# Performance work log

Hardware: AMD Instinct MI355X
Metric: run time of the kernel (lower is better)

## Reference

```python
import jax, jax.numpy as jnp
import numpy as np

N_NODES = 100000
N_EDGES = 1600000
F_IN = 128
HID = 128
N_CLASSES = 32
N_GRAPHS = 512


def _seg_mean(vals, idx, num_segments):
    s = jax.ops.segment_sum(vals, idx, num_segments=num_segments)
    cnt = jax.ops.segment_sum(jnp.ones((vals.shape[0],), vals.dtype), idx, num_segments=num_segments)
    return s / jnp.maximum(cnt, 1.0)[:, None]


def _sage_conv(x, src, dst, Wl, bl, Wr):
    # PyG SAGEConv(mean): out = lin_l(mean_{j in N(i)} x_j) + lin_r(x_i); lin_l has bias, lin_r does not.
    agg = _seg_mean(x[src], dst, N_NODES)          # gather + scatter-mean  [N, d]
    return agg @ Wl.T + bl + x @ Wr.T              # [N, H]


def setup_inputs() -> dict:
    key = jax.random.key(0)
    ks = jax.random.split(key, 16)
    x = jax.random.normal(ks[0], (N_NODES, F_IN), dtype=jnp.float32)
    edge_index = jax.random.randint(ks[1], (2, N_EDGES), 0, N_NODES, dtype=jnp.int64)
    batch = jnp.sort(jax.random.randint(ks[2], (N_NODES,), 0, N_GRAPHS, dtype=jnp.int64))
    sc = 0.05
    params = {
        'Wl0': jax.random.normal(ks[3], (HID, F_IN), jnp.float32) * sc,
        'bl0': jnp.zeros((HID,), jnp.float32),
        'Wr0': jax.random.normal(ks[4], (HID, F_IN), jnp.float32) * sc,
        'Wl1': jax.random.normal(ks[5], (HID, HID), jnp.float32) * sc,
        'bl1': jnp.zeros((HID,), jnp.float32),
        'Wr1': jax.random.normal(ks[6], (HID, HID), jnp.float32) * sc,
        'Wl2': jax.random.normal(ks[7], (HID, HID), jnp.float32) * sc,
        'bl2': jnp.zeros((HID,), jnp.float32),
        'Wr2': jax.random.normal(ks[8], (HID, HID), jnp.float32) * sc,
        'Wlin': jax.random.normal(ks[9], (N_CLASSES, HID), jnp.float32) * sc,
        'blin': jnp.zeros((N_CLASSES,), jnp.float32),
    }
    return {'x': x, 'edge_index': edge_index, 'batch': batch, **params}


def reference(x, edge_index, batch, Wl0, bl0, Wr0, Wl1, bl1, Wr1, Wl2, bl2, Wr2, Wlin, blin):
    src, dst = edge_index[0], edge_index[1]
    # GraphSAGE backbone: relu between layers, no act after last (out_channels set); dropout=identity in eval.
    h = jax.nn.relu(_sage_conv(x, src, dst, Wl0, bl0, Wr0))
    h = jax.nn.relu(_sage_conv(h, src, dst, Wl1, bl1, Wr1))
    h = _sage_conv(h, src, dst, Wl2, bl2, Wr2)
    # global_mean_pool over batch index -> [n_graphs, HID]
    g = _seg_mean(h, batch, N_GRAPHS)
    return g @ Wlin.T + blin  # [n_graphs, n_classes]
```

## Files before the change

kernel.cpp:

```cpp
#include <hip/hip_runtime.h>
#include <hip/hip_bf16.h>


typedef __attribute__((ext_vector_type(8))) short short8v;
typedef __attribute__((ext_vector_type(4))) float f32x4;

__device__ __forceinline__ unsigned short f2bf(float f) {
    __hip_bfloat16 h = __float2bfloat16(f);
    return *reinterpret_cast<unsigned short*>(&h);
}
__device__ __forceinline__ float bf_lo(unsigned u) { return __uint_as_float(u << 16); }
__device__ __forceinline__ float bf_hi(unsigned u) { return __uint_as_float(u & 0xffff0000u); }
__device__ __forceinline__ unsigned packbf(float lo, float hi) {
    return ((unsigned)f2bf(hi) << 16) | f2bf(lo);
}


__global__ void rank_kernel(const int* __restrict__ dst, int* __restrict__ cnt,
                            unsigned short* __restrict__ rank, int nE) {
    int e = blockIdx.x * blockDim.x + threadIdx.x;
    if (e < nE) {
        int r = atomicAdd(&cnt[dst[e]], 1);
        rank[e] = (unsigned short)r;
    }
}

__global__ void scan1_kernel(const int* __restrict__ deg, int* __restrict__ rowptr,
                             int* __restrict__ bsum, int n) {
    __shared__ int s[1024];
    int lid = threadIdx.x;
    int i = blockIdx.x * 1024 + lid;
    int v = (i < n) ? deg[i] : 0;
    s[lid] = v;
    __syncthreads();
    #pragma unroll
    for (int off = 1; off < 1024; off <<= 1) {
        int t = (lid >= off) ? s[lid - off] : 0;
        __syncthreads();
        s[lid] += t;
        __syncthreads();
    }
    if (i < n) rowptr[i] = s[lid] - v;
    if (lid == 0) bsum[blockIdx.x] = s[1023];
}

__global__ void scan2_kernel(int* __restrict__ bsum, int nb) {
    __shared__ int s[1024];
    int lid = threadIdx.x;
    int v = (lid < nb) ? bsum[lid] : 0;
    s[lid] = v;
    __syncthreads();
    #pragma unroll
    for (int off = 1; off < 1024; off <<= 1) {
        int t = (lid >= off) ? s[lid - off] : 0;
        __syncthreads();
        s[lid] += t;
        __syncthreads();
    }
    if (lid < nb) bsum[lid] = s[lid] - v;
}

__global__ void scan3_kernel(int* __restrict__ rowptr, const int* __restrict__ bsum,
                             int n, int nE) {
    int i = blockIdx.x * blockDim.x + threadIdx.x;
    if (i < n) rowptr[i] += bsum[i >> 10];
    if (i == 0) rowptr[n] = nE;
}

__global__ void scatter_rank_kernel(const int* __restrict__ src, const int* __restrict__ dst,
                                    const unsigned short* __restrict__ rank,
                                    const int* __restrict__ rowptr,
                                    int* __restrict__ esrc, int nE, int lo, int hi) {
    int e = blockIdx.x * blockDim.x + threadIdx.x;
    if (e < nE) {
        int d = dst[e];
        if (d >= lo && d < hi) {
            esrc[rowptr[d] + (int)rank[e]] = src[e];
        }
    }
}


__global__ void cvt_kernel(const float* __restrict__ in, unsigned short* __restrict__ out, int n4) {
    int i = blockIdx.x * blockDim.x + threadIdx.x;
    if (i < n4) {
        float4 v = ((const float4*)in)[i];
        ushort4 o;
        o.x = f2bf(v.x); o.y = f2bf(v.y); o.z = f2bf(v.z); o.w = f2bf(v.w);
        ((ushort4*)out)[i] = o;
    }
}

__global__ void cvt6_kernel(const float* __restrict__ w0, const float* __restrict__ w1,
                            const float* __restrict__ w2, const float* __restrict__ w3,
                            const float* __restrict__ w4, const float* __restrict__ w5,
                            unsigned short* __restrict__ o0, unsigned short* __restrict__ o1,
                            unsigned short* __restrict__ o2, unsigned short* __restrict__ o3,
                            unsigned short* __restrict__ o4, unsigned short* __restrict__ o5,
                            int n4) {
    const float* in; unsigned short* out;
    switch (blockIdx.y) {
        case 0: in = w0; out = o0; break;
        case 1: in = w1; out = o1; break;
        case 2: in = w2; out = o2; break;
        case 3: in = w3; out = o3; break;
        case 4: in = w4; out = o4; break;
        default: in = w5; out = o5; break;
    }
    int i = blockIdx.x * blockDim.x + threadIdx.x;
    if (i < n4) {
        float4 v = ((const float4*)in)[i];
        ushort4 o;
        o.x = f2bf(v.x); o.y = f2bf(v.y); o.z = f2bf(v.z); o.w = f2bf(v.w);
        ((ushort4*)out)[i] = o;
    }
}


__global__ void aggregate_kernel(const unsigned short* __restrict__ h,
                                 const int* __restrict__ rowptr,
                                 const int* __restrict__ esrc,
                                 unsigned short* __restrict__ agg, int n) {
    int wave = (blockIdx.x * blockDim.x + threadIdx.x) >> 6;
    int lane = threadIdx.x & 63;
    if (wave >= n) return;
    int beg = rowptr[wave], end = rowptr[wave + 1];
    int q  = lane >> 4;
    int c0 = (lane & 15) * 8;
    float s0=0.f,s1=0.f,s2=0.f,s3=0.f,s4=0.f,s5=0.f,s6=0.f,s7=0.f;
    int j = beg + q;
    for (; j + 4 < end; j += 8) {
        int r0 = esrc[j], r1 = esrc[j + 4];
        uint4 v0 = *(const uint4*)&h[(size_t)r0 * 128 + c0];
        uint4 v1 = *(const uint4*)&h[(size_t)r1 * 128 + c0];
        s0 += bf_lo(v0.x); s1 += bf_hi(v0.x); s2 += bf_lo(v0.y); s3 += bf_hi(v0.y);
        s4 += bf_lo(v0.z); s5 += bf_hi(v0.z); s6 += bf_lo(v0.w); s7 += bf_hi(v0.w);
        s0 += bf_lo(v1.x); s1 += bf_hi(v1.x); s2 += bf_lo(v1.y); s3 += bf_hi(v1.y);
        s4 += bf_lo(v1.z); s5 += bf_hi(v1.z); s6 += bf_lo(v1.w); s7 += bf_hi(v1.w);
    }
    if (j < end) {
        int r0 = esrc[j];
        uint4 v0 = *(const uint4*)&h[(size_t)r0 * 128 + c0];
        s0 += bf_lo(v0.x); s1 += bf_hi(v0.x); s2 += bf_lo(v0.y); s3 += bf_hi(v0.y);
        s4 += bf_lo(v0.z); s5 += bf_hi(v0.z); s6 += bf_lo(v0.w); s7 += bf_hi(v0.w);
    }
    s0 += __shfl_xor(s0, 16); s0 += __shfl_xor(s0, 32);
    s1 += __shfl_xor(s1, 16); s1 += __shfl_xor(s1, 32);
    s2 += __shfl_xor(s2, 16); s2 += __shfl_xor(s2, 32);
    s3 += __shfl_xor(s3, 16); s3 += __shfl_xor(s3, 32);
    s4 += __shfl_xor(s4, 16); s4 += __shfl_xor(s4, 32);
    s5 += __shfl_xor(s5, 16); s5 += __shfl_xor(s5, 32);
    s6 += __shfl_xor(s6, 16); s6 += __shfl_xor(s6, 32);
    s7 += __shfl_xor(s7, 16); s7 += __shfl_xor(s7, 32);
    if (lane < 16) {
        int cnt = end - beg;
        float inv = 1.0f / (float)(cnt > 1 ? cnt : 1);
        uint4 o;
        o.x = packbf(s0 * inv, s1 * inv);
        o.y = packbf(s2 * inv, s3 * inv);
        o.z = packbf(s4 * inv, s5 * inv);
        o.w = packbf(s6 * inv, s7 * inv);
        *(uint4*)&agg[(size_t)wave * 128 + c0] = o;
    }
}


__launch_bounds__(256)
__global__ void sage_gemm_mfma(const unsigned short* __restrict__ A,
                               const unsigned short* __restrict__ H,
                               const unsigned short* __restrict__ Wl,
                               const unsigned short* __restrict__ Wr,
                               const float* __restrict__ bl,
                               unsigned short* __restrict__ out, int n, int relu) {
    int tid  = threadIdx.x;
    int lane = tid & 63;
    int w    = tid >> 6;
    int wm   = w >> 1, wn = w & 1;
    int br   = blockIdx.x * 128 + wm * 64;
    int bc   = wn * 64;
    int lrow = lane & 15;
    int lk   = (lane >> 4) * 8;

    f32x4 acc[4][4] = {};

    #pragma unroll
    for (int half = 0; half < 2; ++half) {
        const unsigned short* X = half ? H : A;
        const unsigned short* W = half ? Wr : Wl;
        const unsigned short* xp[4];
        const unsigned short* wp[4];
        #pragma unroll
        for (int mb = 0; mb < 4; ++mb) {
            int r = br + mb * 16 + lrow;
            if (r >= n) r = n - 1;
            xp[mb] = X + (size_t)r * 128 + lk;
        }
        #pragma unroll
        for (int nb = 0; nb < 4; ++nb)
            wp[nb] = W + (size_t)(bc + nb * 16 + lrow) * 128 + lk;

        #pragma unroll
        for (int ks = 0; ks < 4; ++ks) {
            short8v a[4], b[4];
            #pragma unroll
            for (int mb = 0; mb < 4; ++mb) a[mb] = *(const short8v*)(xp[mb] + ks * 32);
            #pragma unroll
            for (int nb = 0; nb < 4; ++nb) b[nb] = *(const short8v*)(wp[nb] + ks * 32);
            #pragma unroll
            for (int mb = 0; mb < 4; ++mb)
                #pragma unroll
                for (int nb = 0; nb < 4; ++nb)
                    acc[mb][nb] = __builtin_amdgcn_mfma_f32_16x16x32_bf16(
                        a[mb], b[nb], acc[mb][nb], 0, 0, 0);
        }
    }

    int ccol  = lane & 15;
    int crow4 = (lane >> 4) * 4;
    float bv[4];
    #pragma unroll
    for (int nb = 0; nb < 4; ++nb) bv[nb] = bl[bc + nb * 16 + ccol];

    #pragma unroll
    for (int mb = 0; mb < 4; ++mb) {
        #pragma unroll
        for (int r = 0; r < 4; ++r) {
            int row = br + mb * 16 + crow4 + r;
            if (row < n) {
                #pragma unroll
                for (int nb = 0; nb < 4; ++nb) {
                    int col = bc + nb * 16 + ccol;
                    float v = acc[mb][nb][r] + bv[nb];
                    if (relu && v < 0.f) v = 0.f;
                    out[(size_t)row * 128 + col] = f2bf(v);
                }
            }
        }
    }
}


__device__ __forceinline__ int lbound(const int* __restrict__ a, int n, int v) {
    int lo = 0, hi = n;
    while (lo < hi) { int m = (lo + hi) >> 1; if (a[m] < v) lo = m + 1; else hi = m; }
    return lo;
}

__launch_bounds__(1024)
__global__ void pool_kernel(const unsigned short* __restrict__ h, const int* __restrict__ batch,
                            float* __restrict__ g, int n) {
    __shared__ float red[16][128];
    int b  = blockIdx.x;
    int rg = threadIdx.x >> 6;
    int cp = threadIdx.x & 63;
    int lo = lbound(batch, n, b);
    int hi = lbound(batch, n, b + 1);
    float s0 = 0.f, s1 = 0.f;
    for (int i = lo + rg; i < hi; i += 16) {
        unsigned v = *(const unsigned*)&h[(size_t)i * 128 + cp * 2];
        s0 += bf_lo(v); s1 += bf_hi(v);
    }
    red[rg][cp * 2]     = s0;
    red[rg][cp * 2 + 1] = s1;
    __syncthreads();
    #pragma unroll
    for (int off = 8; off >= 1; off >>= 1) {
        if (rg < off) {
            red[rg][cp * 2]     += red[rg + off][cp * 2];
            red[rg][cp * 2 + 1] += red[rg + off][cp * 2 + 1];
        }
        __syncthreads();
    }
    if (rg == 0) {
        int cnt = hi - lo;
        float inv = 1.0f / (float)(cnt > 1 ? cnt : 1);
        g[(size_t)b * 128 + cp * 2]     = red[0][cp * 2] * inv;
        g[(size_t)b * 128 + cp * 2 + 1] = red[0][cp * 2 + 1] * inv;
    }
}

__global__ void final_kernel(const float* __restrict__ g, const float* __restrict__ Wlin,
                             const float* __restrict__ blin, float* __restrict__ out, int total) {
    int gid = blockIdx.x * blockDim.x + threadIdx.x;
    if (gid >= total) return;
    int b = gid >> 5;
    int j = gid & 31;
    const float* gr = &g[(size_t)b * 128];
    const float* wr = &Wlin[(size_t)j * 128];
    float s = blin[j];
    #pragma unroll 4
    for (int c = 0; c < 128; ++c) s += gr[c] * wr[c];
    out[gid] = s;
}

extern "C" void kernel_launch(void* const* d_in, const int* in_sizes, int n_in,
                              void* d_out, int out_size, void* d_ws, size_t ws_size,
                              hipStream_t stream) {
    const float* x      = (const float*)d_in[0];
    const int*   eidx   = (const int*)d_in[1];
    const int*   batch  = (const int*)d_in[2];
    const float* Wl[3]  = {(const float*)d_in[3], (const float*)d_in[6], (const float*)d_in[9]};
    const float* bl[3]  = {(const float*)d_in[4], (const float*)d_in[7], (const float*)d_in[10]};
    const float* Wr[3]  = {(const float*)d_in[5], (const float*)d_in[8], (const float*)d_in[11]};
    const float* Wlin   = (const float*)d_in[12];
    const float* blin   = (const float*)d_in[13];
    float* out = (float*)d_out;

    const int N = in_sizes[0] / 128;
    const int E = in_sizes[1] / 2;
    const int G = out_size / 32;

    const int* esrc_in = eidx;
    const int* edst_in = eidx + E;

    char* w = (char*)d_ws;
    auto carve = [&](size_t bytes) { char* p = w; w += (bytes + 255) & ~(size_t)255; return p; };
    unsigned short* xbf  = (unsigned short*)carve((size_t)N * 128 * 2);
    unsigned short* hA   = (unsigned short*)carve((size_t)N * 128 * 2);
    unsigned short* hB   = (unsigned short*)carve((size_t)N * 128 * 2);
    unsigned short* agg  = (unsigned short*)carve((size_t)N * 128 * 2);
    unsigned short* Wbf[6];
    for (int i = 0; i < 6; ++i) Wbf[i] = (unsigned short*)carve((size_t)128 * 128 * 2);
    float* g      = (float*)carve((size_t)G * 128 * 4);
    int*   cnt    = (int*)carve((size_t)N * 4);
    int*   rowptr = (int*)carve((size_t)(N + 1) * 4);
    int*   bsum   = (int*)carve(1024 * 4);
    int*   esrc   = (int*)carve((size_t)E * 4);
    unsigned short* rank = (unsigned short*)carve((size_t)E * 2);
    (void)ws_size; (void)n_in;

    hipMemsetAsync(cnt, 0, (size_t)N * 4, stream);
    int egrid = (E + 255) / 256;
    hipLaunchKernelGGL(rank_kernel, dim3(egrid), dim3(256), 0, stream, edst_in, cnt, rank, E);
    int nchunks = (N + 1023) / 1024;
    hipLaunchKernelGGL(scan1_kernel, dim3(nchunks), dim3(1024), 0, stream, cnt, rowptr, bsum, N);
    hipLaunchKernelGGL(scan2_kernel, dim3(1), dim3(1024), 0, stream, bsum, nchunks);
    int ngrid = (N + 255) / 256;
    hipLaunchKernelGGL(scan3_kernel, dim3(ngrid), dim3(256), 0, stream, rowptr, bsum, N, E);
    const int NPASS = 4;
    int chunk = (N + NPASS - 1) / NPASS;
    for (int p = 0; p < NPASS; ++p) {
        int lo = p * chunk;
        int hi = lo + chunk < N ? lo + chunk : N;
        hipLaunchKernelGGL(scatter_rank_kernel, dim3(egrid), dim3(256), 0, stream,
                           esrc_in, edst_in, rank, rowptr, esrc, E, lo, hi);
    }

    int x4 = N * 128 / 4;
    hipLaunchKernelGGL(cvt_kernel, dim3((x4 + 255) / 256), dim3(256), 0, stream, x, xbf, x4);
    int w4 = 128 * 128 / 4;
    hipLaunchKernelGGL(cvt6_kernel, dim3((w4 + 255) / 256, 6), dim3(256), 0, stream,
                       Wl[0], Wr[0], Wl[1], Wr[1], Wl[2], Wr[2],
                       Wbf[0], Wbf[1], Wbf[2], Wbf[3], Wbf[4], Wbf[5], w4);

    int agrid = (N + 3) / 4;
    int ggrid = (N + 127) / 128;
    const unsigned short* hin = xbf;
    unsigned short* houts[3] = {hA, hB, hA};
    for (int l = 0; l < 3; ++l) {
        hipLaunchKernelGGL(aggregate_kernel, dim3(agrid), dim3(256), 0, stream,
                           hin, rowptr, esrc, agg, N);
        hipLaunchKernelGGL(sage_gemm_mfma, dim3(ggrid), dim3(256), 0, stream,
                           agg, hin, Wbf[2*l], Wbf[2*l+1], bl[l], houts[l], N, (l < 2) ? 1 : 0);
        hin = houts[l];
    }

    hipLaunchKernelGGL(pool_kernel, dim3(G), dim3(1024), 0, stream, hin, batch, g, N);
    int fgrid = (out_size + 255) / 256;
    hipLaunchKernelGGL(final_kernel, dim3(fgrid), dim3(256), 0, stream, g, Wlin, blin, out, out_size);
}
```

Before: 432.5 us.

## Replace global atomic edge ranking with LDS-chunked histogram and segment offsets

Global atomics on per-node counters for CSR construction are replaced by a two-level counting sort. Blocks histogram their edge slices into shared-memory node chunks, a per-node pass turns the slice counts into exclusive offsets and degrees, and the scatter adds slice offset plus local rank. The aim is to remove contended global atomics. In exchange it adds a counts buffer sized chunks x slices x chunk, makes each block re-read its whole edge slice once per node chunk, and lowers the scatter pass count from 4 to 2.

```diff
diff --git a/kernel.cpp b/kernel.cpp
--- a/kernel.cpp
+++ b/kernel.cpp
@@ -4,6 +4,9 @@
 
 typedef __attribute__((ext_vector_type(8))) short short8v;
 typedef __attribute__((ext_vector_type(4))) float f32x4;
+
+#define RK_CH 12544
+#define RK_NS 64
 
 __device__ __forceinline__ unsigned short f2bf(float f) {
     __hip_bfloat16 h = __float2bfloat16(f);
@@ -16,13 +19,69 @@
 }
 
 
-__global__ void rank_kernel(const int* __restrict__ dst, int* __restrict__ cnt,
-                            unsigned short* __restrict__ rank, int nE) {
-    int e = blockIdx.x * blockDim.x + threadIdx.x;
-    if (e < nE) {
-        int r = atomicAdd(&cnt[dst[e]], 1);
-        rank[e] = (unsigned short)r;
-    }
+__launch_bounds__(256)
+__global__ void rank_hist_kernel(const int* __restrict__ dst,
+                                 unsigned short* __restrict__ rank16,
+                                 unsigned short* __restrict__ counts16,
+                                 int nE, int nChunk, int es) {
+    __shared__ unsigned cnt[RK_CH];
+    int s = blockIdx.x / nChunk;
+    int c = blockIdx.x % nChunk;
+    int lo = c * RK_CH;
+    for (int i = threadIdx.x; i < RK_CH; i += 256) cnt[i] = 0u;
+    __syncthreads();
+
+    int ebeg = s * es;
+    int eend = ebeg + es; if (eend > nE) eend = nE;
+
+    if (ebeg < eend) {
+        if ((((size_t)dst) & 15) == 0) {
+            int nvec = (eend - ebeg) >> 2;
+            for (int g = threadIdx.x; g < nvec; g += 256) {
+                int e = ebeg + g * 4;
+                int4 d4 = *(const int4*)&dst[e];
+                unsigned dc;
+                dc = (unsigned)(d4.x - lo);
+                if (dc < RK_CH) rank16[e]     = (unsigned short)atomicAdd(&cnt[dc], 1u);
+                dc = (unsigned)(d4.y - lo);
+                if (dc < RK_CH) rank16[e + 1] = (unsigned short)atomicAdd(&cnt[dc], 1u);
+                dc = (unsigned)(d4.z - lo);
+                if (dc < RK_CH) rank16[e + 2] = (unsigned short)atomicAdd(&cnt[dc], 1u);
+                dc = (unsigned)(d4.w - lo);
+                if (dc < RK_CH) rank16[e + 3] = (unsigned short)atomicAdd(&cnt[dc], 1u);
+            }
+            for (int e = ebeg + (nvec << 2) + threadIdx.x; e < eend; e += 256) {
+                unsigned dc = (unsigned)(dst[e] - lo);
+                if (dc < RK_CH) rank16[e] = (unsigned short)atomicAdd(&cnt[dc], 1u);
+            }
+        } else {
+            for (int e = ebeg + threadIdx.x; e < eend; e += 256) {
+                unsigned dc = (unsigned)(dst[e] - lo);
+                if (dc < RK_CH) rank16[e] = (unsigned short)atomicAdd(&cnt[dc], 1u);
+            }
+        }
+    }
+    __syncthreads();
+    size_t base = ((size_t)(c * RK_NS + s)) * RK_CH;
+    for (int i = threadIdx.x; i < RK_CH; i += 256)
+        counts16[base + i] = (unsigned short)cnt[i];
+}
+
+__global__ void seg_offsets_kernel(unsigned short* __restrict__ counts16,
+                                   int* __restrict__ deg, int n) {
+    int d = blockIdx.x * blockDim.x + threadIdx.x;
+    if (d >= n) return;
+    int c = d / RK_CH;
+    int i = d - c * RK_CH;
+    size_t base = ((size_t)c * RK_NS) * RK_CH + i;
+    unsigned run = 0;
+    for (int s = 0; s < RK_NS; ++s) {
+        size_t idx = base + (size_t)s * RK_CH;
+        unsigned v = counts16[idx];
+        counts16[idx] = (unsigned short)run;
+        run += v;
+    }
+    deg[d] = (int)run;
 }
 
 __global__ void scan1_kernel(const int* __restrict__ deg, int* __restrict__ rowptr,
@@ -67,17 +126,21 @@
     if (i == 0) rowptr[n] = nE;
 }
 
-__global__ void scatter_rank_kernel(const int* __restrict__ src, const int* __restrict__ dst,
-                                    const unsigned short* __restrict__ rank,
-                                    const int* __restrict__ rowptr,
-                                    int* __restrict__ esrc, int nE, int lo, int hi) {
+__global__ void scatter2_kernel(const int* __restrict__ src, const int* __restrict__ dst,
+                                const unsigned short* __restrict__ rank16,
+                                const unsigned short* __restrict__ counts16,
+                                const int* __restrict__ rowptr,
+                                int* __restrict__ esrc, int nE, int es, int lo, int hi) {
     int e = blockIdx.x * blockDim.x + threadIdx.x;
-    if (e < nE) {
-        int d = dst[e];
-        if (d >= lo && d < hi) {
-            esrc[rowptr[d] + (int)rank[e]] = src[e];
-        }
-    }
+    if (e >= nE) return;
+    int d = dst[e];
+    if (d < lo || d >= hi) return;
+    int s = e / es;
+    int c = d / RK_CH;
+    int i = d - c * RK_CH;
+    int pos = rowptr[d] + (int)counts16[((size_t)(c * RK_NS + s)) * RK_CH + i]
+                        + (int)rank16[e];
+    esrc[pos] = src[e];
 }
 
 
@@ -322,28 +385,33 @@
     unsigned short* Wbf[6];
     for (int i = 0; i < 6; ++i) Wbf[i] = (unsigned short*)carve((size_t)128 * 128 * 2);
     float* g      = (float*)carve((size_t)G * 128 * 4);
-    int*   cnt    = (int*)carve((size_t)N * 4);
+    int*   deg    = (int*)carve((size_t)N * 4);
     int*   rowptr = (int*)carve((size_t)(N + 1) * 4);
     int*   bsum   = (int*)carve(1024 * 4);
     int*   esrc   = (int*)carve((size_t)E * 4);
-    unsigned short* rank = (unsigned short*)carve((size_t)E * 2);
+    unsigned short* rank16   = (unsigned short*)carve((size_t)E * 2);
+    int nChunk = (N + RK_CH - 1) / RK_CH;
+    unsigned short* counts16 = (unsigned short*)carve((size_t)nChunk * RK_NS * RK_CH * 2);
     (void)ws_size; (void)n_in;
 
-    hipMemsetAsync(cnt, 0, (size_t)N * 4, stream);
+    int es = (((E + RK_NS - 1) / RK_NS) + 3) & ~3;
+    hipLaunchKernelGGL(rank_hist_kernel, dim3(nChunk * RK_NS), dim3(256), 0, stream,
+                       edst_in, rank16, counts16, E, nChunk, es);
+    int ngrid = (N + 255) / 256;
+    hipLaunchKernelGGL(seg_offsets_kernel, dim3(ngrid), dim3(256), 0, stream,
+                       counts16, deg, N);
+    int nchunks = (N + 1023) / 1024;
+    hipLaunchKernelGGL(scan1_kernel, dim3(nchunks), dim3(1024), 0, stream, deg, rowptr, bsum, N);
+    hipLaunchKernelGGL(scan2_kernel, dim3(1), dim3(1024), 0, stream, bsum, nchunks);
+    hipLaunchKernelGGL(scan3_kernel, dim3(ngrid), dim3(256), 0, stream, rowptr, bsum, N, E);
     int egrid = (E + 255) / 256;
-    hipLaunchKernelGGL(rank_kernel, dim3(egrid), dim3(256), 0, stream, edst_in, cnt, rank, E);
-    int nchunks = (N + 1023) / 1024;
-    hipLaunchKernelGGL(scan1_kernel, dim3(nchunks), dim3(1024), 0, stream, cnt, rowptr, bsum, N);
-    hipLaunchKernelGGL(scan2_kernel, dim3(1), dim3(1024), 0, stream, bsum, nchunks);
-    int ngrid = (N + 255) / 256;
-    hipLaunchKernelGGL(scan3_kernel, dim3(ngrid), dim3(256), 0, stream, rowptr, bsum, N, E);
-    const int NPASS = 4;
+    const int NPASS = 2;
     int chunk = (N + NPASS - 1) / NPASS;
     for (int p = 0; p < NPASS; ++p) {
         int lo = p * chunk;
         int hi = lo + chunk < N ? lo + chunk : N;
-        hipLaunchKernelGGL(scatter_rank_kernel, dim3(egrid), dim3(256), 0, stream,
-                           esrc_in, edst_in, rank, rowptr, esrc, E, lo, hi);
+        hipLaunchKernelGGL(scatter2_kernel, dim3(egrid), dim3(256), 0, stream,
+                           esrc_in, edst_in, rank16, counts16, rowptr, esrc, E, es, lo, hi);
     }
 
     int x4 = N * 128 / 4;
```

After: 398.0 us. 8.0% less time.
